# Optimization experiments

Hardware: AMD Instinct MI355X
Metric: run time of the kernel (lower is better)

## Reference

```python
import jax, jax.numpy as jnp
import numpy as np

DEGREES = [1, 2, 3]
NUM_SEGMENTS = len(DEGREES)


def setup_inputs() -> dict:
    key = jax.random.key(0)
    B = 4_000_000
    m_tot = sum(2 * l + 1 for l in DEGREES)  # 15
    sphc = jax.random.normal(key, (B, m_tot), dtype=jnp.float32)
    # Clebsch-Gordan diagonal for l_out=0: a constant per degree block
    # (real-basis value 1/sqrt(2l+1) per m-component), tiled per degree,
    # mirroring the cg_rep buffer built in __init__.
    cg_rep = jnp.concatenate([
        jnp.full((2 * l + 1,), 1.0 / np.sqrt(2 * l + 1), dtype=jnp.float32)
        for l in DEGREES
    ])
    # segment n repeated (2*degrees[n]+1) times -> contiguous sorted blocks
    segment_ids = jnp.concatenate([
        jnp.full((2 * l + 1,), n, dtype=jnp.int32)
        for n, l in enumerate(DEGREES)
    ])
    return {"sphc": sphc, "cg_rep": cg_rep, "segment_ids": segment_ids}


def reference(sphc, cg_rep, segment_ids):
    # (B, m_tot): fused elementwise square * CG weight
    weighted = sphc * sphc * cg_rep[None, :]
    # Per-degree block reduction along the feature axis. Segments are
    # contiguous and sorted, so segment_sum over the transposed feature
    # axis is a direct tiled block reduction (no atomic scatter needed).
    out = jax.ops.segment_sum(
        weighted.T, segment_ids, num_segments=NUM_SEGMENTS,
        indices_are_sorted=True,
    ).T  # (B, num_segments)
    return out
```

## Files before the change

kernel.cpp:

```cpp
#include <hip/hip_runtime.h>
#include <hip/hip_bf16.h>


constexpr int M = 15;
constexpr int NSEG = 3;
constexpr int RPB = 256;
constexpr int IN_F4 = RPB * M / 4;
constexpr int OUT_F4 = RPB * NSEG / 4;

__global__ __launch_bounds__(RPB)
void l0_contract_kernel(const float* __restrict__ sphc,
                        const float* __restrict__ cg_rep,
                        float* __restrict__ out,
                        int B) {
    __shared__ float s_in[RPB * M];
    __shared__ float s_out[RPB * NSEG];

    const int tid = threadIdx.x;
    const long long rowStart = (long long)blockIdx.x * RPB;
    const long long rowsLeft = (long long)B - rowStart;
    const int rowsHere = rowsLeft >= RPB ? RPB : (int)rowsLeft;

    if (rowsHere == RPB) {
        const float4* __restrict__ g4 =
            (const float4*)(sphc + rowStart * M);
        float4* l4 = (float4*)s_in;
#pragma unroll
        for (int i = tid; i < IN_F4; i += RPB) {
            l4[i] = g4[i];
        }
    } else {
        const int n = rowsHere * M;
        const float* g = sphc + rowStart * M;
        for (int i = tid; i < n; i += RPB) s_in[i] = g[i];
    }
    __syncthreads();

    const float c1 = cg_rep[0];
    const float c2 = cg_rep[3];
    const float c3 = cg_rep[8];

    if (tid < rowsHere) {
        const float* r = s_in + tid * M;
        float a = r[0] * r[0] + r[1] * r[1] + r[2] * r[2];
        float b = r[3] * r[3] + r[4] * r[4] + r[5] * r[5]
                + r[6] * r[6] + r[7] * r[7];
        float c = r[8] * r[8] + r[9] * r[9] + r[10] * r[10]
                + r[11] * r[11] + r[12] * r[12] + r[13] * r[13]
                + r[14] * r[14];
        s_out[tid * NSEG + 0] = a * c1;
        s_out[tid * NSEG + 1] = b * c2;
        s_out[tid * NSEG + 2] = c * c3;
    }
    __syncthreads();

    if (rowsHere == RPB) {
        const float4* lo4 = (const float4*)s_out;
        float4* o4 = (float4*)(out + rowStart * NSEG);
        if (tid < OUT_F4) o4[tid] = lo4[tid];
    } else {
        const int n = rowsHere * NSEG;
        float* o = out + rowStart * NSEG;
        for (int i = tid; i < n; i += RPB) o[i] = s_out[i];
    }
}

extern "C" void kernel_launch(void* const* d_in, const int* in_sizes, int n_in,
                              void* d_out, int out_size, void* d_ws, size_t ws_size,
                              hipStream_t stream) {
    const float* sphc   = (const float*)d_in[0];
    const float* cg_rep = (const float*)d_in[1];
    float* out = (float*)d_out;

    const int B = in_sizes[0] / M;
    const int grid = (B + RPB - 1) / RPB;

    l0_contract_kernel<<<grid, RPB, 0, stream>>>(sphc, cg_rep, out, B);
}
```

Before: 335.9 us.

## Replace LDS staging with direct per-thread vector loads of four rows

Each thread now loads four whole rows (15 float4s) straight from global memory into registers, computes the three segment sums, and writes three float4 outputs with nontemporal stores. This removes the shared-memory staging buffers and both block barriers. In exchange, each thread's loads are strided by 240 bytes, so a warp's accesses are less contiguous than the old cooperative loads, and register use per thread goes up.

```diff
diff --git a/kernel.cpp b/kernel.cpp
--- a/kernel.cpp
+++ b/kernel.cpp
@@ -4,64 +4,66 @@
 
 constexpr int M = 15;
 constexpr int NSEG = 3;
-constexpr int RPB = 256;
-constexpr int IN_F4 = RPB * M / 4;
-constexpr int OUT_F4 = RPB * NSEG / 4;
+constexpr int RPT = 4;
+constexpr int BLK = 256;
 
-__global__ __launch_bounds__(RPB)
-void l0_contract_kernel(const float* __restrict__ sphc,
+typedef float f32x4 __attribute__((ext_vector_type(4)));
+
+__global__ __launch_bounds__(BLK)
+void l0_contract_direct(const float* __restrict__ sphc,
                         const float* __restrict__ cg_rep,
                         float* __restrict__ out,
                         int B) {
-    __shared__ float s_in[RPB * M];
-    __shared__ float s_out[RPB * NSEG];
-
-    const int tid = threadIdx.x;
-    const long long rowStart = (long long)blockIdx.x * RPB;
-    const long long rowsLeft = (long long)B - rowStart;
-    const int rowsHere = rowsLeft >= RPB ? RPB : (int)rowsLeft;
-
-    if (rowsHere == RPB) {
-        const float4* __restrict__ g4 =
-            (const float4*)(sphc + rowStart * M);
-        float4* l4 = (float4*)s_in;
-#pragma unroll
-        for (int i = tid; i < IN_F4; i += RPB) {
-            l4[i] = g4[i];
-        }
-    } else {
-        const int n = rowsHere * M;
-        const float* g = sphc + rowStart * M;
-        for (int i = tid; i < n; i += RPB) s_in[i] = g[i];
-    }
-    __syncthreads();
+    const long long gid = (long long)blockIdx.x * BLK + threadIdx.x;
+    const long long r0 = gid * RPT;
+    if (r0 >= B) return;
 
     const float c1 = cg_rep[0];
     const float c2 = cg_rep[3];
     const float c3 = cg_rep[8];
 
-    if (tid < rowsHere) {
-        const float* r = s_in + tid * M;
-        float a = r[0] * r[0] + r[1] * r[1] + r[2] * r[2];
-        float b = r[3] * r[3] + r[4] * r[4] + r[5] * r[5]
-                + r[6] * r[6] + r[7] * r[7];
-        float c = r[8] * r[8] + r[9] * r[9] + r[10] * r[10]
-                + r[11] * r[11] + r[12] * r[12] + r[13] * r[13]
-                + r[14] * r[14];
-        s_out[tid * NSEG + 0] = a * c1;
-        s_out[tid * NSEG + 1] = b * c2;
-        s_out[tid * NSEG + 2] = c * c3;
-    }
-    __syncthreads();
+    if (r0 + RPT <= B) {
+        const f32x4* __restrict__ g4 = (const f32x4*)sphc + gid * (M * RPT / 4);
+        f32x4 v[M * RPT / 4];
+#pragma unroll
+        for (int i = 0; i < M * RPT / 4; ++i) v[i] = g4[i];
+        const float* f = (const float*)v;
 
-    if (rowsHere == RPB) {
-        const float4* lo4 = (const float4*)s_out;
-        float4* o4 = (float4*)(out + rowStart * NSEG);
-        if (tid < OUT_F4) o4[tid] = lo4[tid];
+        f32x4 o[RPT * NSEG / 4];
+        float* of = (float*)o;
+#pragma unroll
+        for (int r = 0; r < RPT; ++r) {
+            const float* x = f + r * M;
+            float a = x[0] * x[0] + x[1] * x[1] + x[2] * x[2];
+            float b = x[3] * x[3] + x[4] * x[4] + x[5] * x[5]
+                    + x[6] * x[6] + x[7] * x[7];
+            float c = x[8] * x[8] + x[9] * x[9] + x[10] * x[10]
+                    + x[11] * x[11] + x[12] * x[12] + x[13] * x[13]
+                    + x[14] * x[14];
+            of[r * NSEG + 0] = a * c1;
+            of[r * NSEG + 1] = b * c2;
+            of[r * NSEG + 2] = c * c3;
+        }
+
+        f32x4* o4 = (f32x4*)out + gid * (RPT * NSEG / 4);
+#pragma unroll
+        for (int i = 0; i < RPT * NSEG / 4; ++i) {
+            __builtin_nontemporal_store(o[i], &o4[i]);
+        }
     } else {
-        const int n = rowsHere * NSEG;
-        float* o = out + rowStart * NSEG;
-        for (int i = tid; i < n; i += RPB) o[i] = s_out[i];
+        for (long long r = r0; r < B; ++r) {
+            const float* x = sphc + r * M;
+            float a = x[0] * x[0] + x[1] * x[1] + x[2] * x[2];
+            float b = x[3] * x[3] + x[4] * x[4] + x[5] * x[5]
+                    + x[6] * x[6] + x[7] * x[7];
+            float c = x[8] * x[8] + x[9] * x[9] + x[10] * x[10]
+                    + x[11] * x[11] + x[12] * x[12] + x[13] * x[13]
+                    + x[14] * x[14];
+            float* o = out + r * NSEG;
+            __builtin_nontemporal_store(a * c1, &o[0]);
+            __builtin_nontemporal_store(b * c2, &o[1]);
+            __builtin_nontemporal_store(c * c3, &o[2]);
+        }
     }
 }
 
@@ -73,7 +75,8 @@
     float* out = (float*)d_out;
 
     const int B = in_sizes[0] / M;
-    const int grid = (B + RPB - 1) / RPB;
+    const long long nThreads = ((long long)B + RPT - 1) / RPT;
+    const int grid = (int)((nThreads + BLK - 1) / BLK);
 
-    l0_contract_kernel<<<grid, RPB, 0, stream>>>(sphc, cg_rep, out, B);
+    l0_contract_direct<<<grid, BLK, 0, stream>>>(sphc, cg_rep, out, B);
 }
```

After: 345.4 us. +2.8%, slower.
